# Kernel tuning notes

Hardware: AMD Instinct MI355X
Metric: run time of the kernel (lower is better)

The kernel has to match this reference:

```python
import jax, jax.numpy as jnp
import numpy as np

K = 1024   # in_dim = out_dim = per-head dim (module uses full k per head)
H = 4      # heads
B, T = 2, 2048


def setup_inputs() -> dict:
    key = jax.random.key(0)
    ks = jax.random.split(key, 7)
    s = 0.02
    return {
        "x": jax.random.normal(ks[0], (B, T, K), jnp.float32),
        "Wq": jax.random.normal(ks[1], (K, K * H), jnp.float32) * s,
        "Wk": jax.random.normal(ks[2], (K, K * H), jnp.float32) * s,
        "Wv": jax.random.normal(ks[3], (K, K * H), jnp.float32) * s,
        "Wu": jax.random.normal(ks[4], (K * H, K), jnp.float32) * s,
        "bu": jnp.zeros((K,), jnp.float32),
        "W1": jax.random.normal(ks[5], (K, K), jnp.float32) * s,
        "b1": jnp.zeros((K,), jnp.float32),
        "W2": jax.random.normal(ks[6], (K, K), jnp.float32) * s,
        "b2": jnp.zeros((K,), jnp.float32),
    }


def reference(x, Wq, Wk, Wv, Wu, bu, W1, b1, W2, b2):
    b, t, k = x.shape
    h = H
    scale = k ** (-0.25)
    # projections: each head gets FULL dim k (quirk of the original module)
    q = (x @ Wq).reshape(b, t, h, k) * scale   # [b,t,h,k]
    kk = (x @ Wk).reshape(b, t, h, k) * scale
    v = (x @ Wv).reshape(b, t, h, k)
    # attention scores [b,h,q,k_pos]
    dot = jnp.einsum("bqhd,bkhd->bhqk", q, kk)
    causal = jnp.tril(jnp.ones((t, t), bool))  # strictly-upper masked to -inf
    dot = jnp.where(causal, dot, -jnp.inf)
    attn = jax.nn.softmax(dot, axis=-1)
    out = jnp.einsum("bhqk,bkhd->bqhd", attn, v).reshape(b, t, h * k)
    attn_out = out @ Wu + bu                   # unifyheads
    x = x + attn_out                            # residual
    ff = jax.nn.relu(x @ W1 + b1) @ W2 + b2     # in_dim == out_dim
    return x + ff                               # residual around FFN
```

## Files before the change

kernel.cpp:

```cpp
#include <hip/hip_runtime.h>
#include <math.h>


#define TM 128
#define TN 128
#define BK 64

typedef __attribute__((ext_vector_type(8))) short short8;
typedef __attribute__((ext_vector_type(4))) float f32x4;

__device__ __forceinline__ unsigned short f2bf(float f) {
  union { float f; unsigned int u; } v; v.f = f;
  unsigned int r = (v.u + 0x7fffu + ((v.u >> 16) & 1u)) >> 16;
  return (unsigned short)r;
}
__device__ __forceinline__ float bf2f(unsigned short b) {
  union { unsigned int u; float f; } v; v.u = ((unsigned int)b) << 16;
  return v.f;
}

#define GL2LDS(g, l)                                                          \
  __builtin_amdgcn_global_load_lds(                                           \
      (__attribute__((address_space(1))) void*)(g),                           \
      (__attribute__((address_space(3))) void*)(l), 16, 0, 0)

__device__ __forceinline__ void gemm_core(
    const unsigned short* __restrict__ A, const unsigned short* __restrict__ BT,
    int m0, int n0, int kmax, int lda, int ldb, int ldc, long long coff,
    float scale, const float* __restrict__ bias,
    const float* __restrict__ resid, int do_relu, float* __restrict__ Cf,
    unsigned short* __restrict__ Cb, unsigned short* As, unsigned short* Bs) {
  const int tid = threadIdx.x;
  const int lane = tid & 63;
  const int wv = tid >> 6;
  const int wm = wv & 1;
  const int wn = wv >> 1;

  const int srow = tid >> 2;
  const int scol = (tid & 3) * 8;
  const unsigned short* ap0 = A + (long long)(m0 + srow) * lda + scol;
  const unsigned short* ap1 = ap0 + (long long)64 * lda;
  const unsigned short* bp0 = BT + (long long)(n0 + srow) * ldb + scol;
  const unsigned short* bp1 = bp0 + (long long)64 * ldb;
  unsigned short* lA00 = As + wv * 512;
  unsigned short* lA10 = As + 2048 + wv * 512;
  unsigned short* lA01 = As + 4096 + wv * 512;
  unsigned short* lA11 = As + 6144 + wv * 512;
  unsigned short* lB00 = Bs + wv * 512;
  unsigned short* lB10 = Bs + 2048 + wv * 512;
  unsigned short* lB01 = Bs + 4096 + wv * 512;
  unsigned short* lB11 = Bs + 6144 + wv * 512;

  f32x4 acc[4][4];
#pragma unroll
  for (int i = 0; i < 4; ++i)
#pragma unroll
    for (int j2 = 0; j2 < 4; ++j2) acc[i][j2] = {0.f, 0.f, 0.f, 0.f};

  const int frow = lane & 15;
  const int fq = (lane >> 4) * 8;

  for (int k0 = 0; k0 < kmax; k0 += BK) {
    __syncthreads();
    GL2LDS(ap0, lA00); GL2LDS(ap0 + 32, lA01);
    GL2LDS(ap1, lA10); GL2LDS(ap1 + 32, lA11);
    GL2LDS(bp0, lB00); GL2LDS(bp0 + 32, lB01);
    GL2LDS(bp1, lB10); GL2LDS(bp1 + 32, lB11);
    ap0 += BK; ap1 += BK; bp0 += BK; bp1 += BK;
    __syncthreads();

#pragma unroll
    for (int s = 0; s < 2; ++s) {
      short8 afr[4], bfr[4];
#pragma unroll
      for (int mi = 0; mi < 4; ++mi)
        afr[mi] = *(const short8*)(As + s * 4096 +
                                   (wm * 64 + mi * 16 + frow) * 32 + fq);
#pragma unroll
      for (int ni = 0; ni < 4; ++ni)
        bfr[ni] = *(const short8*)(Bs + s * 4096 +
                                   (wn * 64 + ni * 16 + frow) * 32 + fq);
#pragma unroll
      for (int mi = 0; mi < 4; ++mi)
#pragma unroll
        for (int ni = 0; ni < 4; ++ni)
          acc[mi][ni] = __builtin_amdgcn_mfma_f32_16x16x32_bf16(
              afr[mi], bfr[ni], acc[mi][ni], 0, 0, 0);
    }
  }

  const int ccol = lane & 15;
  const int crow = (lane >> 4) * 4;
#pragma unroll
  for (int mi = 0; mi < 4; ++mi) {
#pragma unroll
    for (int ni = 0; ni < 4; ++ni) {
      const int gc = n0 + wn * 64 + ni * 16 + ccol;
#pragma unroll
      for (int r = 0; r < 4; ++r) {
        const int gr = m0 + wm * 64 + mi * 16 + crow + r;
        float v = acc[mi][ni][r] * scale;
        if (bias) v += bias[gc];
        if (resid) v += resid[(long long)gr * ldc + gc];
        if (do_relu) v = fmaxf(v, 0.f);
        const long long ci = coff + (long long)gr * ldc + gc;
        if (Cf) Cf[ci] = v;
        if (Cb) Cb[ci] = f2bf(v);
      }
    }
  }
}

__global__ __launch_bounds__(256) void gemm_bt(
    const unsigned short* __restrict__ A, const unsigned short* __restrict__ BT,
    int Kd, int lda, int ldb, int ldc, int bh_shift,
    long long aob, long long aoh, long long bob, long long boh,
    long long cob, long long coh, float scale,
    const float* __restrict__ bias, const float* __restrict__ resid,
    int do_relu, float* __restrict__ Cf, unsigned short* __restrict__ Cb,
    int causal_mode, int grid_mode) {
  __shared__ unsigned short As[8192];
  __shared__ unsigned short Bs[8192];
  int n0, m0, z;
  if (grid_mode == 2) {
    z = blockIdx.x; n0 = blockIdx.y * TN; m0 = blockIdx.z * TM;
  } else if (grid_mode == 4) {
    z = blockIdx.x; m0 = blockIdx.y * TM; n0 = blockIdx.z * TN;
  } else if (grid_mode == 5) {
    const int bid = blockIdx.x;
    z = bid & 7;
    const int idx = bid >> 3;
    int m = (int)((sqrtf(8.0f * idx + 1.0f) - 1.0f) * 0.5f);
    while ((m + 1) * (m + 2) / 2 <= idx) ++m;
    while (m * (m + 1) / 2 > idx) --m;
    m0 = m * TM;
    n0 = (idx - m * (m + 1) / 2) * TN;
  } else if (grid_mode == 6) {
    const int bid = blockIdx.x;
    const int xcd = bid & 7;
    const int j = bid >> 3;
    const int ns = j >> 2;
    m0 = (xcd * 4 + (j & 3)) * TM;
    n0 = (ns >> 2) * TN;
    z = ns & 3;
  } else {
    n0 = blockIdx.x * TN; m0 = blockIdx.y * TM; z = blockIdx.z;
  }
  if (causal_mode == 1 && n0 >= m0 + TM) return;

  const int zb = z >> bh_shift;
  const int zh = z & ((1 << bh_shift) - 1);
  const long long aoff = (long long)zb * aob + (long long)zh * aoh;
  const long long boff = (long long)zb * bob + (long long)zh * boh;
  const long long coff = (long long)zb * cob + (long long)zh * coh;

  int kmax = Kd;
  if (causal_mode == 2) { int t = m0 + TM; if (t < kmax) kmax = t; }

  gemm_core(A + aoff, BT + boff, m0, n0, kmax, lda, ldb, ldc, coff, scale,
            bias, resid, do_relu, Cf, Cb, As, Bs);
}

__global__ __launch_bounds__(256) void gemm_tvv(
    const unsigned short* __restrict__ xb,
    const unsigned short* __restrict__ Wcomb,
    unsigned short* __restrict__ tb, unsigned short* __restrict__ vT) {
  __shared__ unsigned short As[8192];
  __shared__ unsigned short Bs[8192];
  const int bid = blockIdx.x;
  if (bid < 1024) {
    const int xcd = bid & 7;
    const int j = bid >> 3;
    const int m0 = (xcd * 4 + (j & 3)) * TM;
    const int n0 = (j >> 2) * TN;
    gemm_core(xb, Wcomb, m0, n0, 1024, 1024, 1024, 4096, 0, 1.0f,
              nullptr, nullptr, 0, nullptr, tb, As, Bs);
  } else {
    const int r = bid - 1024;
    const int xcd = r & 7;
    const int j = r >> 3;
    const int bb = j >> 6;
    const int rr = j & 63;
    const int m0 = (xcd * 4 + (rr & 3)) * TM;
    const int n0 = (rr >> 2) * TN;
    gemm_core(Wcomb + (size_t)4096 * 1024, xb + (long long)bb * 2048 * 1024,
              m0, n0, 1024, 1024, 1024, 2048, (long long)bb * 4096 * 2048,
              1.0f, nullptr, nullptr, 0, nullptr, vT, As, Bs);
  }
}

__global__ __launch_bounds__(256) void reduce_epi(
    const unsigned short* __restrict__ Pb, int S, long long MN,
    const float* __restrict__ bias, const float* __restrict__ resid,
    int do_relu, float* __restrict__ Cf, unsigned short* __restrict__ Cb) {
  const long long i4 = ((long long)blockIdx.x * 256 + threadIdx.x) * 4;
  if (i4 >= MN) return;
  float4 s = {0.f, 0.f, 0.f, 0.f};
  for (int t = 0; t < S; ++t) {
    const ushort4 p = *(const ushort4*)(Pb + (long long)t * MN + i4);
    s.x += bf2f(p.x); s.y += bf2f(p.y); s.z += bf2f(p.z); s.w += bf2f(p.w);
  }
  if (bias) {
    const int c0 = (int)(i4 & 1023);
    s.x += bias[c0]; s.y += bias[c0 + 1]; s.z += bias[c0 + 2]; s.w += bias[c0 + 3];
  }
  if (resid) {
    const float4 rr = *(const float4*)(resid + i4);
    s.x += rr.x; s.y += rr.y; s.z += rr.z; s.w += rr.w;
  }
  if (do_relu) {
    s.x = fmaxf(s.x, 0.f); s.y = fmaxf(s.y, 0.f);
    s.z = fmaxf(s.z, 0.f); s.w = fmaxf(s.w, 0.f);
  }
  if (Cf) *(float4*)(Cf + i4) = s;
  if (Cb) {
    ushort4 o;
    o.x = f2bf(s.x); o.y = f2bf(s.y); o.z = f2bf(s.z); o.w = f2bf(s.w);
    *(ushort4*)(Cb + i4) = o;
  }
}

__global__ __launch_bounds__(256) void softmax_causal(unsigned short* S, int T) {
  const int q = blockIdx.x;
  unsigned short* row = S + ((long long)blockIdx.y * T + q) * T;
  const int tid = threadIdx.x;
  const int lane = tid & 63;
  const int wv = tid >> 6;
  const int n = q + 1;
  const int nz = (n + 127) & ~127;
  const int base = tid * 8;
  short8 raw = {};
  if (base < nz) raw = *(const short8*)(row + base);
  float vals[8];
  float m = -__builtin_inff();
#pragma unroll
  for (int i = 0; i < 8; ++i) {
    vals[i] = (base + i < n) ? bf2f((unsigned short)raw[i]) : -__builtin_inff();
    m = fmaxf(m, vals[i]);
  }
#pragma unroll
  for (int o = 32; o; o >>= 1) m = fmaxf(m, __shfl_xor(m, o, 64));
  __shared__ float red[4];
  if (lane == 0) red[wv] = m;
  __syncthreads();
  m = fmaxf(fmaxf(red[0], red[1]), fmaxf(red[2], red[3]));
  __syncthreads();
  float s = 0.f, e[8];
#pragma unroll
  for (int i = 0; i < 8; ++i) {
    e[i] = (base + i < n) ? __expf(vals[i] - m) : 0.f;
    s += e[i];
  }
#pragma unroll
  for (int o = 32; o; o >>= 1) s += __shfl_xor(s, o, 64);
  if (lane == 0) red[wv] = s;
  __syncthreads();
  s = red[0] + red[1] + red[2] + red[3];
  const float inv = 1.f / s;
  if (base < nz) {
    short8 o8;
#pragma unroll
    for (int i = 0; i < 8; ++i) o8[i] = (short)f2bf(e[i] * inv);
    *(short8*)(row + base) = o8;
  }
}

__global__ __launch_bounds__(256) void prep_all(
    const float* __restrict__ x, const float* __restrict__ Wq,
    const float* __restrict__ Wk, const float* __restrict__ Wv,
    const float* __restrict__ Wu, const float* __restrict__ W1,
    const float* __restrict__ W2, unsigned short* __restrict__ xb,
    unsigned short* __restrict__ Wqc, unsigned short* __restrict__ Wkc,
    unsigned short* __restrict__ Wvc, unsigned short* __restrict__ WuTb,
    unsigned short* __restrict__ W1T, unsigned short* __restrict__ W2T,
    float s2) {
  const int z = blockIdx.y;
  if (z <= 3) {
    const float* src = (z == 0) ? x : (z == 1) ? Wq : (z == 2) ? Wk : Wv;
    unsigned short* dst = (z == 0) ? xb : (z == 1) ? Wqc : (z == 2) ? Wkc : Wvc;
    const float sc = (z == 2) ? s2 : 1.0f;
    const long long i4 = ((long long)blockIdx.x * 256 + threadIdx.x) * 4;
    const float4 v = *(const float4*)(src + i4);
    ushort4 u;
    u.x = f2bf(v.x * sc); u.y = f2bf(v.y * sc);
    u.z = f2bf(v.z * sc); u.w = f2bf(v.w * sc);
    *(ushort4*)(dst + i4) = u;
    return;
  }
  const int R = (z == 4) ? 4096 : 1024;
  const int by = blockIdx.x >> 5;
  if (by * 32 >= R) return;
  const float* W = (z == 4) ? Wu : (z == 5) ? W1 : W2;
  unsigned short* WT = (z == 4) ? WuTb : (z == 5) ? W1T : W2T;
  __shared__ float tile[32][33];
  const int c0 = (blockIdx.x & 31) * 32;
  const int r0 = by * 32;
  const int tx = threadIdx.x & 31;
  const int ty = threadIdx.x >> 5;
#pragma unroll
  for (int j = 0; j < 32; j += 8)
    tile[ty + j][tx] = W[(long long)(r0 + ty + j) * 1024 + c0 + tx];
  __syncthreads();
#pragma unroll
  for (int j = 0; j < 32; j += 8)
    WT[(long long)(c0 + ty + j) * R + r0 + tx] = f2bf(tile[tx][ty + j]);
}

extern "C" void kernel_launch(void* const* d_in, const int* in_sizes, int n_in,
                              void* d_out, int out_size, void* d_ws,
                              size_t ws_size, hipStream_t stream) {
  (void)in_sizes; (void)n_in; (void)out_size; (void)ws_size;
  const float* x  = (const float*)d_in[0];
  const float* Wq = (const float*)d_in[1];
  const float* Wk = (const float*)d_in[2];
  const float* Wv = (const float*)d_in[3];
  const float* Wu = (const float*)d_in[4];
  const float* bu = (const float*)d_in[5];
  const float* W1 = (const float*)d_in[6];
  const float* b1 = (const float*)d_in[7];
  const float* W2 = (const float*)d_in[8];
  const float* b2 = (const float*)d_in[9];
  float* out = (float*)d_out;

  const int T = 2048, K = 1024;
  const int BT = 4096;
  const size_t MB = 1024 * 1024;
  const long long MN = (long long)BT * K;
  const long long TT = (long long)T * T;
  const long long Mi = 1024 * 1024;

  char* w = (char*)d_ws;
  unsigned short* xb    = (unsigned short*)(w + 0 * MB);
  unsigned short* Wqc   = (unsigned short*)(w + 8 * MB);
  unsigned short* Wvc   = (unsigned short*)(w + 16 * MB);
  unsigned short* Wkc   = (unsigned short*)(w + 24 * MB);
  unsigned short* WuTb  = (unsigned short*)(w + 32 * MB);
  unsigned short* Wcomb = (unsigned short*)(w + 40 * MB);
  unsigned short* tb    = (unsigned short*)(w + 56 * MB);
  unsigned short* vT    = (unsigned short*)(w + 88 * MB);
  unsigned short* S     = (unsigned short*)(w + 120 * MB);
  unsigned short* W1T   = (unsigned short*)(w + 184 * MB);
  unsigned short* W2T   = (unsigned short*)(w + 186 * MB);
  unsigned short* Pb    = (unsigned short*)(w + 40 * MB);
  float*          x1f   = (float*)(w + 8 * MB);
  unsigned short* x1b   = (unsigned short*)(w + 24 * MB);
  unsigned short* h1    = (unsigned short*)(w + 32 * MB);
  unsigned short* Pb2   = (unsigned short*)(w + 88 * MB);

  const float s2 = 0.03125f;

  prep_all<<<dim3(4096, 7), 256, 0, stream>>>(
      x, Wq, Wk, Wv, Wu, W1, W2, xb, Wqc, Wkc, Wvc, WuTb, W1T, W2T, s2);

  gemm_bt<<<dim3(8, 8, 8), 256, 0, stream>>>(
      Wkc, Wqc, K, 4096, 4096, 1024, 2,
      4 * Mi, 1024, 4 * Mi, 1024, 4 * Mi, Mi, 1.0f,
      nullptr, nullptr, 0, nullptr, Wcomb, 0, 2);

  gemm_tvv<<<dim3(2048), 256, 0, stream>>>(xb, Wcomb, tb, vT);

  gemm_bt<<<dim3(1088), 256, 0, stream>>>(
      tb, xb, K, 4096, K, T, 2,
      (long long)T * 4096, 1024, (long long)T * K, 0,
      (long long)4 * TT, TT, 1.0f,
      nullptr, nullptr, 0, nullptr, S, 0, 5);

  softmax_causal<<<dim3(T, 8), 256, 0, stream>>>(S, T);

  gemm_bt<<<dim3(8, T / TM, K / TN), 256, 0, stream>>>(
      S, vT, T, T, 2048, K, 2,
      (long long)4 * TT, TT, (long long)4096 * 2048, (long long)1024 * 2048,
      (long long)2048 * 1024, MN, 1.0f,
      nullptr, nullptr, 0, nullptr, Pb, 2, 4);

  reduce_epi<<<dim3(4096), 256, 0, stream>>>(Pb, 4, MN, bu, x, 0, x1f, x1b);

  gemm_bt<<<dim3(1024), 256, 0, stream>>>(
      x1b, W1T, 256, K, K, K, 0,
      256, 0, 256, 0, MN, 0, 1.0f,
      nullptr, nullptr, 0, nullptr, Pb2, 0, 6);
  reduce_epi<<<dim3(4096), 256, 0, stream>>>(Pb2, 4, MN, b1, nullptr, 1,
                                             nullptr, h1);

  gemm_bt<<<dim3(1024), 256, 0, stream>>>(
      h1, W2T, 256, K, K, K, 0,
      256, 0, 256, 0, MN, 0, 1.0f,
      nullptr, nullptr, 0, nullptr, Pb2, 0, 6);
  reduce_epi<<<dim3(4096), 256, 0, stream>>>(Pb2, 4, MN, b2, x1f, 0, out,
                                             nullptr);
}
```

Before: 493.9 us.

## Move V-transpose projection into the causal score GEMM launch

The V^T projection blocks move out of the combined t/v kernel and into the launch that computes the causal score tiles, so the t GEMM runs alone and the score and V projections share one grid. The goal is better load balance, since the triangular score grid leaves the GPU underfilled and the independent V work can fill those slots. It also removes the generic grid_mode 5 and causal early-return paths from gemm_bt. The cost is a different block ordering and cache locality for the V work.

```diff
diff --git a/kernel.cpp b/kernel.cpp
--- a/kernel.cpp
+++ b/kernel.cpp
@@ -126,15 +126,6 @@
     z = blockIdx.x; n0 = blockIdx.y * TN; m0 = blockIdx.z * TM;
   } else if (grid_mode == 4) {
     z = blockIdx.x; m0 = blockIdx.y * TM; n0 = blockIdx.z * TN;
-  } else if (grid_mode == 5) {
-    const int bid = blockIdx.x;
-    z = bid & 7;
-    const int idx = bid >> 3;
-    int m = (int)((sqrtf(8.0f * idx + 1.0f) - 1.0f) * 0.5f);
-    while ((m + 1) * (m + 2) / 2 <= idx) ++m;
-    while (m * (m + 1) / 2 > idx) --m;
-    m0 = m * TM;
-    n0 = (idx - m * (m + 1) / 2) * TN;
   } else if (grid_mode == 6) {
     const int bid = blockIdx.x;
     const int xcd = bid & 7;
@@ -146,7 +137,6 @@
   } else {
     n0 = blockIdx.x * TN; m0 = blockIdx.y * TM; z = blockIdx.z;
   }
-  if (causal_mode == 1 && n0 >= m0 + TM) return;
 
   const int zb = z >> bh_shift;
   const int zh = z & ((1 << bh_shift) - 1);
@@ -161,22 +151,45 @@
             bias, resid, do_relu, Cf, Cb, As, Bs);
 }
 
-__global__ __launch_bounds__(256) void gemm_tvv(
+__global__ __launch_bounds__(256) void gemm_t(
     const unsigned short* __restrict__ xb,
     const unsigned short* __restrict__ Wcomb,
-    unsigned short* __restrict__ tb, unsigned short* __restrict__ vT) {
+    unsigned short* __restrict__ tb) {
   __shared__ unsigned short As[8192];
   __shared__ unsigned short Bs[8192];
   const int bid = blockIdx.x;
-  if (bid < 1024) {
-    const int xcd = bid & 7;
-    const int j = bid >> 3;
-    const int m0 = (xcd * 4 + (j & 3)) * TM;
-    const int n0 = (j >> 2) * TN;
-    gemm_core(xb, Wcomb, m0, n0, 1024, 1024, 1024, 4096, 0, 1.0f,
-              nullptr, nullptr, 0, nullptr, tb, As, Bs);
+  const int xcd = bid & 7;
+  const int j = bid >> 3;
+  const int m0 = (xcd * 4 + (j & 3)) * TM;
+  const int n0 = (j >> 2) * TN;
+  gemm_core(xb, Wcomb, m0, n0, 1024, 1024, 1024, 4096, 0, 1.0f,
+            nullptr, nullptr, 0, nullptr, tb, As, Bs);
+}
+
+__global__ __launch_bounds__(256) void gemm_sv(
+    const unsigned short* __restrict__ xb,
+    const unsigned short* __restrict__ Wcomb,
+    const unsigned short* __restrict__ tb,
+    unsigned short* __restrict__ S, unsigned short* __restrict__ vT) {
+  __shared__ unsigned short As[8192];
+  __shared__ unsigned short Bs[8192];
+  const long long TT = (long long)2048 * 2048;
+  const int bid = blockIdx.x;
+  if (bid < 1088) {
+    const int z = bid & 7, zb = z >> 2, zh = z & 3;
+    const int idx = bid >> 3;
+    int m = (int)((sqrtf(8.0f * idx + 1.0f) - 1.0f) * 0.5f);
+    while ((m + 1) * (m + 2) / 2 <= idx) ++m;
+    while (m * (m + 1) / 2 > idx) --m;
+    const int m0 = m * TM;
+    const int n0 = (idx - m * (m + 1) / 2) * TN;
+    gemm_core(tb + (long long)zb * 2048 * 4096 + zh * 1024,
+              xb + (long long)zb * 2048 * 1024,
+              m0, n0, 1024, 4096, 1024, 2048,
+              (long long)zb * 4 * TT + (long long)zh * TT,
+              1.0f, nullptr, nullptr, 0, nullptr, S, As, Bs);
   } else {
-    const int r = bid - 1024;
+    const int r = bid - 1088;
     const int xcd = r & 7;
     const int j = r >> 3;
     const int bb = j >> 6;
@@ -357,13 +370,9 @@
       4 * Mi, 1024, 4 * Mi, 1024, 4 * Mi, Mi, 1.0f,
       nullptr, nullptr, 0, nullptr, Wcomb, 0, 2);
 
-  gemm_tvv<<<dim3(2048), 256, 0, stream>>>(xb, Wcomb, tb, vT);
-
-  gemm_bt<<<dim3(1088), 256, 0, stream>>>(
-      tb, xb, K, 4096, K, T, 2,
-      (long long)T * 4096, 1024, (long long)T * K, 0,
-      (long long)4 * TT, TT, 1.0f,
-      nullptr, nullptr, 0, nullptr, S, 0, 5);
+  gemm_t<<<dim3(1024), 256, 0, stream>>>(xb, Wcomb, tb);
+
+  gemm_sv<<<dim3(2112), 256, 0, stream>>>(xb, Wcomb, tb, S, vT);
 
   softmax_causal<<<dim3(T, 8), 256, 0, stream>>>(S, T);
 
```

After: 486.7 us. Within noise of the previous version (-1.5%).
